# Optimization experiments

Hardware: AMD Instinct MI355X
Metric: run time of the kernel (lower is better)

The kernel has to match this reference:

```python
import jax, jax.numpy as jnp
import numpy as np

N_NODES = 100000
N_EDGES = 1600000
F_IN = 64
CONVS = [128, 128, 64]
DECODER_HID = 128
N_CLASSES = 2


def _glorot(key, shape):
    fan_in = shape[1]
    lim = 1.0 / np.sqrt(fan_in)
    return jax.random.uniform(key, shape, jnp.float32, -lim, lim)


def setup_inputs() -> dict:
    key = jax.random.key(0)
    ks = jax.random.split(key, 16)
    x = jax.random.normal(ks[0], (N_NODES, F_IN), jnp.float32)
    edge_index = jax.random.randint(ks[1], (2, N_EDGES), 0, N_NODES, jnp.int32)
    dims = [F_IN] + CONVS  # [64,128,128,64]
    inp = {"x": x, "edge_index": edge_index}
    ki = 2
    for i in range(len(CONVS)):
        d_in, d_out = dims[i], dims[i + 1]
        inp[f"Wl{i}"] = _glorot(ks[ki], (d_out, d_in)); ki += 1
        inp[f"bl{i}"] = jnp.zeros((d_out,), jnp.float32)
        inp[f"Wr{i}"] = _glorot(ks[ki], (d_out, d_in)); ki += 1
    inp["Wd1"] = _glorot(ks[ki], (DECODER_HID, CONVS[-1])); ki += 1
    inp["bd1"] = jnp.zeros((DECODER_HID,), jnp.float32)
    inp["Wd2"] = _glorot(ks[ki], (N_CLASSES, DECODER_HID)); ki += 1
    inp["bd2"] = jnp.zeros((N_CLASSES,), jnp.float32)
    return inp


def _sage_conv(x, src, dst, inv_deg, Wl, bl, Wr):
    # gather source features per edge, scatter-mean onto destinations
    msg = x[src]                                          # [E, F]
    agg = jax.ops.segment_sum(msg, dst, num_segments=N_NODES)
    agg = agg * inv_deg[:, None]                          # mean aggregation
    # out = lin_l(mean_neighbors) + lin_r(x_self)
    return agg @ Wl.T + bl + x @ Wr.T


def reference(x, edge_index, Wl0, bl0, Wr0, Wl1, bl1, Wr1, Wl2, bl2, Wr2, Wd1, bd1, Wd2, bd2):
    src = edge_index[0]
    dst = edge_index[1]
    deg = jax.ops.segment_sum(jnp.ones((src.shape[0],), x.dtype), dst, num_segments=N_NODES)
    inv_deg = jnp.where(deg > 0, 1.0 / jnp.maximum(deg, 1.0), 0.0)
    params = [(Wl0, bl0, Wr0), (Wl1, bl1, Wr1), (Wl2, bl2, Wr2)]
    h = x
    for i, (Wl, bl, Wr) in enumerate(params):
        h = _sage_conv(h, src, dst, inv_deg, Wl, bl, Wr)
        if i != len(params) - 1:
            h = jax.nn.relu(h)
    # decoder: ReLU -> Linear(64,128) -> ReLU -> Linear(128,2)
    h = jax.nn.relu(h)
    h = jax.nn.relu(h @ Wd1.T + bd1)
    return h @ Wd2.T + bd2
```

## Files before the change

kernel.cpp:

```cpp
#include <hip/hip_runtime.h>
#include <cstdint>
#include <cstddef>

#define NN 100000
#define NE 1600000
#define BSH 9
#define NBUCK 196
#define P3_CHUNK 8192
#define P3_BLOCKS 196

typedef __attribute__((ext_vector_type(8))) short short8;
typedef __attribute__((ext_vector_type(4))) float f32x4;


__device__ inline unsigned pack_split(float v) {
    unsigned u = __builtin_bit_cast(unsigned, v);
    unsigned hi = (u + 0x7fffu + ((u >> 16) & 1u)) >> 16;
    float vh = __builtin_bit_cast(float, hi << 16);
    float r = v - vh;
    unsigned u2 = __builtin_bit_cast(unsigned, r);
    unsigned lo = (u2 + 0x7fffu + ((u2 >> 16) & 1u)) >> 16;
    return hi | (lo << 16);
}

__device__ inline unsigned short rnb(float v) {
    unsigned u = __builtin_bit_cast(unsigned, v);
    return (unsigned short)((u + 0x7fffu + ((u >> 16) & 1u)) >> 16);
}

__device__ inline float bf2f(unsigned short u) {
    return __builtin_bit_cast(float, (unsigned)u << 16);
}


__global__ __launch_bounds__(256) void k_zero_small(int* p, int n) {
    for (int i = threadIdx.x; i < n; i += 256) p[i] = 0;
}

__global__ __launch_bounds__(256) void k_hist(const int* __restrict__ dst, int* __restrict__ bcnt) {
    __shared__ int h[NBUCK];
    const int tid = threadIdx.x;
    if (tid < NBUCK) h[tid] = 0;
    __syncthreads();
    for (int e = blockIdx.x * 256 + tid; e < NE; e += gridDim.x * 256)
        atomicAdd(&h[dst[e] >> BSH], 1);
    __syncthreads();
    if (tid < NBUCK) atomicAdd(&bcnt[tid], h[tid]);
}

__global__ __launch_bounds__(256) void k_bscan(const int* __restrict__ bcnt, int* __restrict__ bstart,
                                               int* __restrict__ gcur) {
    __shared__ int sh[256];
    const int t = threadIdx.x;
    int v = (t < NBUCK) ? bcnt[t] : 0;
    sh[t] = v;
    __syncthreads();
    for (int off = 1; off < 256; off <<= 1) {
        int u = 0;
        if (t >= off) u = sh[t - off];
        __syncthreads();
        sh[t] += u;
        __syncthreads();
    }
    int excl = sh[t] - v;
    if (t < NBUCK) { bstart[t] = excl; gcur[t] = excl; }
    if (t == 0) bstart[NBUCK] = NE;
}

__global__ __launch_bounds__(256) void k_partition(const int* __restrict__ srce, const int* __restrict__ dste,
                                                   int* __restrict__ gcur, int* __restrict__ tmp) {
    __shared__ int h[NBUCK], lstart[NBUCK], gbase[NBUCK], scn[256];
    __shared__ int s_pack[P3_CHUNK];
    __shared__ int s_gad[P3_CHUNK];
    const int tid = threadIdx.x;
    const int base = blockIdx.x * P3_CHUNK;
    if (tid < NBUCK) h[tid] = 0;
    __syncthreads();
    int rank[P3_CHUNK / 256];
#pragma unroll
    for (int i = 0; i < P3_CHUNK / 256; i++) {
        int idx = base + i * 256 + tid;
        if (idx < NE) rank[i] = atomicAdd(&h[dste[idx] >> BSH], 1);
    }
    __syncthreads();
    int hv = (tid < NBUCK) ? h[tid] : 0;
    if (tid < NBUCK) gbase[tid] = atomicAdd(&gcur[tid], hv);
    scn[tid] = hv;
    __syncthreads();
    for (int off = 1; off < 256; off <<= 1) {
        int u = 0;
        if (tid >= off) u = scn[tid - off];
        __syncthreads();
        scn[tid] += u;
        __syncthreads();
    }
    if (tid < NBUCK) lstart[tid] = scn[tid] - hv;
    __syncthreads();
#pragma unroll
    for (int i = 0; i < P3_CHUNK / 256; i++) {
        int idx = base + i * 256 + tid;
        if (idx < NE) {
            int d = dste[idx], s = srce[idx];
            int b = d >> BSH;
            int slot = lstart[b] + rank[i];
            s_pack[slot] = (s << BSH) | (d & ((1 << BSH) - 1));
            s_gad[slot] = gbase[b] + rank[i];
        }
    }
    __syncthreads();
    int chunkN = NE - base;
    if (chunkN > P3_CHUNK) chunkN = P3_CHUNK;
#pragma unroll
    for (int i = 0; i < P3_CHUNK / 256; i++) {
        int slot = i * 256 + tid;
        if (slot < chunkN) tmp[s_gad[slot]] = s_pack[slot];
    }
}

__global__ __launch_bounds__(256) void k_bucket(const int* __restrict__ tmp, const int* __restrict__ bstart,
                                                int* __restrict__ row_ptr, int* __restrict__ col,
                                                float* __restrict__ invd) {
    __shared__ int cnt[512], cur[512], scn[256];
    const int b = blockIdx.x, tid = threadIdx.x;
    const int base = bstart[b];
    const int n = bstart[b + 1] - base;
    cnt[tid] = 0;
    cnt[tid + 256] = 0;
    __syncthreads();
    for (int k = tid; k < n; k += 256) atomicAdd(&cnt[tmp[base + k] & 511], 1);
    __syncthreads();
    int c0 = cnt[2 * tid], c1 = cnt[2 * tid + 1], s = c0 + c1;
    scn[tid] = s;
    __syncthreads();
    for (int off = 1; off < 256; off <<= 1) {
        int u = 0;
        if (tid >= off) u = scn[tid - off];
        __syncthreads();
        scn[tid] += u;
        __syncthreads();
    }
    int excl = scn[tid] - s;
    int node = (b << BSH) + 2 * tid;
    if (node < NN) {
        row_ptr[node] = base + excl;
        invd[node] = c0 ? 1.0f / (float)c0 : 0.0f;
    }
    if (node + 1 < NN) {
        row_ptr[node + 1] = base + excl + c0;
        invd[node + 1] = c1 ? 1.0f / (float)c1 : 0.0f;
    }
    cur[2 * tid] = base + excl;
    cur[2 * tid + 1] = base + excl + c0;
    if (b == 0 && tid == 0) row_ptr[NN] = NE;
    __syncthreads();
    for (int k = tid; k < n; k += 256) {
        int p = tmp[base + k];
        int pos = atomicAdd(&cur[p & 511], 1);
        col[pos] = p >> BSH;
    }
}


__global__ __launch_bounds__(256) void k_xhi(const float* __restrict__ x, unsigned short* __restrict__ Xh) {
    int i = blockIdx.x * 256 + threadIdx.x;
    float4 v = ((const float4*)x)[i];
    ushort4 o = {rnb(v.x), rnb(v.y), rnb(v.z), rnb(v.w)};
    ((ushort4*)Xh)[i] = o;
}

__global__ __launch_bounds__(256) void k_wsplit(const float* __restrict__ Wl0, const float* __restrict__ Wr0,
                                                const float* __restrict__ Wl1, const float* __restrict__ Wr1,
                                                const float* __restrict__ Wl2, const float* __restrict__ Wr2,
                                                const float* __restrict__ Wd1, const float* __restrict__ bl2,
                                                unsigned short* __restrict__ Wh, unsigned short* __restrict__ Wl,
                                                float* __restrict__ biasPQ) {
    int i = blockIdx.x * 256 + threadIdx.x;
    float v = 0.f;
    bool valid = true;
    if (i < 8192) v = Wl0[i];
    else if (i < 16384) v = Wr0[i - 8192];
    else if (i < 32768) v = Wl1[i - 16384];
    else if (i < 49152) v = Wr1[i - 32768];
    else if (i < 57344) v = Wl2[i - 49152];
    else if (i < 65536) v = Wr2[i - 57344];
    else if (i < 73728) v = Wd1[i - 65536];
    else valid = false;
    if (valid) {
        unsigned ps = pack_split(v);
        Wh[i] = (unsigned short)ps;
        Wl[i] = (unsigned short)(ps >> 16);
    }
    if (i >= 73728 && i < 73856) {
        int j = i - 73728;
        biasPQ[j] = (j < 64) ? 0.f : bl2[j - 64];
    }
}


__global__ __launch_bounds__(256) void k_agg64h(const unsigned short* __restrict__ Xh, const int* __restrict__ row_ptr,
                                                const int* __restrict__ col, const float* __restrict__ invd,
                                                unsigned short* __restrict__ Ah, unsigned short* __restrict__ Al) {
    int node = blockIdx.x * 4 + (threadIdx.x >> 6);
    int lane = threadIdx.x & 63;
    int start = row_ptr[node], end = row_ptr[node + 1];
    float a0 = 0.f, a1 = 0.f, a2 = 0.f, a3 = 0.f, a4 = 0.f, a5 = 0.f, a6 = 0.f, a7 = 0.f;
    for (int cs = start; cs < end; cs += 64) {
        int n = end - cs;
        if (n > 64) n = 64;
        int my = (lane < n) ? col[cs + lane] : 0;
        int j = 0;
        for (; j + 8 <= n; j += 8) {
            int s0 = __shfl(my, j + 0), s1 = __shfl(my, j + 1);
            int s2 = __shfl(my, j + 2), s3 = __shfl(my, j + 3);
            int s4 = __shfl(my, j + 4), s5 = __shfl(my, j + 5);
            int s6 = __shfl(my, j + 6), s7 = __shfl(my, j + 7);
            float v0 = bf2f(Xh[(size_t)s0 * 64 + lane]);
            float v1 = bf2f(Xh[(size_t)s1 * 64 + lane]);
            float v2 = bf2f(Xh[(size_t)s2 * 64 + lane]);
            float v3 = bf2f(Xh[(size_t)s3 * 64 + lane]);
            float v4 = bf2f(Xh[(size_t)s4 * 64 + lane]);
            float v5 = bf2f(Xh[(size_t)s5 * 64 + lane]);
            float v6 = bf2f(Xh[(size_t)s6 * 64 + lane]);
            float v7 = bf2f(Xh[(size_t)s7 * 64 + lane]);
            a0 += v0; a1 += v1; a2 += v2; a3 += v3;
            a4 += v4; a5 += v5; a6 += v6; a7 += v7;
        }
        for (; j < n; j++) {
            int s = __shfl(my, j);
            a0 += bf2f(Xh[(size_t)s * 64 + lane]);
        }
    }
    float acc = ((a0 + a1) + (a2 + a3)) + ((a4 + a5) + (a6 + a7));
    unsigned ps = pack_split(acc * invd[node]);
    Ah[(size_t)node * 64 + lane] = (unsigned short)ps;
    Al[(size_t)node * 64 + lane] = (unsigned short)(ps >> 16);
}

__global__ __launch_bounds__(256) void k_agg128h(const unsigned short* __restrict__ Gh, const int* __restrict__ row_ptr,
                                                 const int* __restrict__ col, const float* __restrict__ invd,
                                                 unsigned short* __restrict__ Ah, unsigned short* __restrict__ Al) {
    int node = blockIdx.x * 4 + (threadIdx.x >> 6);
    int lane = threadIdx.x & 63;
    int start = row_ptr[node], end = row_ptr[node + 1];
    float ax0 = 0.f, ax1 = 0.f, ax2 = 0.f, ax3 = 0.f, ax4 = 0.f, ax5 = 0.f, ax6 = 0.f, ax7 = 0.f;
    float ay0 = 0.f, ay1 = 0.f, ay2 = 0.f, ay3 = 0.f, ay4 = 0.f, ay5 = 0.f, ay6 = 0.f, ay7 = 0.f;
    for (int cs = start; cs < end; cs += 64) {
        int n = end - cs;
        if (n > 64) n = 64;
        int my = (lane < n) ? col[cs + lane] : 0;
        int j = 0;
        for (; j + 8 <= n; j += 8) {
            int s0 = __shfl(my, j + 0), s1 = __shfl(my, j + 1);
            int s2 = __shfl(my, j + 2), s3 = __shfl(my, j + 3);
            int s4 = __shfl(my, j + 4), s5 = __shfl(my, j + 5);
            int s6 = __shfl(my, j + 6), s7 = __shfl(my, j + 7);
            unsigned u0 = *(const unsigned*)(Gh + (size_t)s0 * 128 + 2 * lane);
            unsigned u1 = *(const unsigned*)(Gh + (size_t)s1 * 128 + 2 * lane);
            unsigned u2 = *(const unsigned*)(Gh + (size_t)s2 * 128 + 2 * lane);
            unsigned u3 = *(const unsigned*)(Gh + (size_t)s3 * 128 + 2 * lane);
            unsigned u4 = *(const unsigned*)(Gh + (size_t)s4 * 128 + 2 * lane);
            unsigned u5 = *(const unsigned*)(Gh + (size_t)s5 * 128 + 2 * lane);
            unsigned u6 = *(const unsigned*)(Gh + (size_t)s6 * 128 + 2 * lane);
            unsigned u7 = *(const unsigned*)(Gh + (size_t)s7 * 128 + 2 * lane);
            ax0 += bf2f((unsigned short)u0); ay0 += bf2f((unsigned short)(u0 >> 16));
            ax1 += bf2f((unsigned short)u1); ay1 += bf2f((unsigned short)(u1 >> 16));
            ax2 += bf2f((unsigned short)u2); ay2 += bf2f((unsigned short)(u2 >> 16));
            ax3 += bf2f((unsigned short)u3); ay3 += bf2f((unsigned short)(u3 >> 16));
            ax4 += bf2f((unsigned short)u4); ay4 += bf2f((unsigned short)(u4 >> 16));
            ax5 += bf2f((unsigned short)u5); ay5 += bf2f((unsigned short)(u5 >> 16));
            ax6 += bf2f((unsigned short)u6); ay6 += bf2f((unsigned short)(u6 >> 16));
            ax7 += bf2f((unsigned short)u7); ay7 += bf2f((unsigned short)(u7 >> 16));
        }
        for (; j < n; j++) {
            int s = __shfl(my, j);
            unsigned u = *(const unsigned*)(Gh + (size_t)s * 128 + 2 * lane);
            ax0 += bf2f((unsigned short)u);
            ay0 += bf2f((unsigned short)(u >> 16));
        }
    }
    float w = invd[node];
    float sx = (((ax0 + ax1) + (ax2 + ax3)) + ((ax4 + ax5) + (ax6 + ax7))) * w;
    float sy = (((ay0 + ay1) + (ay2 + ay3)) + ((ay4 + ay5) + (ay6 + ay7))) * w;
    unsigned px = pack_split(sx), py = pack_split(sy);
    *(unsigned*)(Ah + (size_t)node * 128 + 2 * lane) = (px & 0xffffu) | (py << 16);
    *(unsigned*)(Al + (size_t)node * 128 + 2 * lane) = (px >> 16) | (py & 0xffff0000u);
}

__global__ __launch_bounds__(256) void k_aggPh(const unsigned short* __restrict__ Ph, const float* __restrict__ Qf,
                                               const int* __restrict__ row_ptr, const int* __restrict__ col,
                                               const float* __restrict__ invd,
                                               unsigned short* __restrict__ Hh, unsigned short* __restrict__ Hl) {
    int node = blockIdx.x * 4 + (threadIdx.x >> 6);
    int lane = threadIdx.x & 63;
    int start = row_ptr[node], end = row_ptr[node + 1];
    float a0 = 0.f, a1 = 0.f, a2 = 0.f, a3 = 0.f, a4 = 0.f, a5 = 0.f, a6 = 0.f, a7 = 0.f;
    for (int cs = start; cs < end; cs += 64) {
        int n = end - cs;
        if (n > 64) n = 64;
        int my = (lane < n) ? col[cs + lane] : 0;
        int j = 0;
        for (; j + 8 <= n; j += 8) {
            int s0 = __shfl(my, j + 0), s1 = __shfl(my, j + 1);
            int s2 = __shfl(my, j + 2), s3 = __shfl(my, j + 3);
            int s4 = __shfl(my, j + 4), s5 = __shfl(my, j + 5);
            int s6 = __shfl(my, j + 6), s7 = __shfl(my, j + 7);
            float v0 = bf2f(Ph[(size_t)s0 * 64 + lane]);
            float v1 = bf2f(Ph[(size_t)s1 * 64 + lane]);
            float v2 = bf2f(Ph[(size_t)s2 * 64 + lane]);
            float v3 = bf2f(Ph[(size_t)s3 * 64 + lane]);
            float v4 = bf2f(Ph[(size_t)s4 * 64 + lane]);
            float v5 = bf2f(Ph[(size_t)s5 * 64 + lane]);
            float v6 = bf2f(Ph[(size_t)s6 * 64 + lane]);
            float v7 = bf2f(Ph[(size_t)s7 * 64 + lane]);
            a0 += v0; a1 += v1; a2 += v2; a3 += v3;
            a4 += v4; a5 += v5; a6 += v6; a7 += v7;
        }
        for (; j < n; j++) {
            int s = __shfl(my, j);
            a0 += bf2f(Ph[(size_t)s * 64 + lane]);
        }
    }
    float acc = ((a0 + a1) + (a2 + a3)) + ((a4 + a5) + (a6 + a7));
    float v = Qf[(size_t)node * 64 + lane] + invd[node] * acc;
    unsigned ps = pack_split(fmaxf(v, 0.f));
    Hh[(size_t)node * 64 + lane] = (unsigned short)ps;
    Hl[(size_t)node * 64 + lane] = (unsigned short)(ps >> 16);
}


#define LA 40

template <int K, int AFMT>
__device__ inline void mgp(const unsigned short* __restrict__ Ah_g, const unsigned short* __restrict__ Al_g,
                           const float* __restrict__ Af_g,
                           const unsigned short* __restrict__ Wh_g, const unsigned short* __restrict__ Wl_g,
                           int m0, unsigned short* sAh, unsigned short* sAl,
                           unsigned short* sBh, unsigned short* sBl,
                           f32x4 (&acc)[4][4], int tid, int wm, int wn, int l15, int quad) {
    const int srow = tid >> 1, sc = (tid & 1) * 16;
#pragma unroll 1
    for (int kt = 0; kt < K; kt += 32) {
        __syncthreads();
        int gr = m0 + srow;
        uint4 h0 = {0, 0, 0, 0}, h1 = {0, 0, 0, 0}, l0 = {0, 0, 0, 0}, l1 = {0, 0, 0, 0};
        if (AFMT == 0) {
            if (gr < NN) {
                const uint4* ph = (const uint4*)(Ah_g + (size_t)gr * K + kt + sc);
                h0 = ph[0]; h1 = ph[1];
                const uint4* pl = (const uint4*)(Al_g + (size_t)gr * K + kt + sc);
                l0 = pl[0]; l1 = pl[1];
            }
        } else {
            if (gr < NN) {
                const float4* pf = (const float4*)(Af_g + (size_t)gr * K + kt + sc);
                float4 f0 = pf[0], f1 = pf[1], f2 = pf[2], f3 = pf[3];
                float fs[16] = {f0.x, f0.y, f0.z, f0.w, f1.x, f1.y, f1.z, f1.w,
                                f2.x, f2.y, f2.z, f2.w, f3.x, f3.y, f3.z, f3.w};
                alignas(16) unsigned short hh[16], ll[16];
#pragma unroll
                for (int i = 0; i < 16; i++) {
                    unsigned ps = pack_split(fs[i]);
                    hh[i] = (unsigned short)ps;
                    ll[i] = (unsigned short)(ps >> 16);
                }
                h0 = *(const uint4*)&hh[0]; h1 = *(const uint4*)&hh[8];
                l0 = *(const uint4*)&ll[0]; l1 = *(const uint4*)&ll[8];
            }
        }
        const uint4* qh = (const uint4*)(Wh_g + srow * K + kt + sc);
        uint4 b0 = qh[0], b1 = qh[1];
        const uint4* ql = (const uint4*)(Wl_g + srow * K + kt + sc);
        uint4 b2 = ql[0], b3 = ql[1];
        *(uint4*)(sAh + srow * LA + sc) = h0; *(uint4*)(sAh + srow * LA + sc + 8) = h1;
        *(uint4*)(sAl + srow * LA + sc) = l0; *(uint4*)(sAl + srow * LA + sc + 8) = l1;
        *(uint4*)(sBh + srow * LA + sc) = b0; *(uint4*)(sBh + srow * LA + sc + 8) = b1;
        *(uint4*)(sBl + srow * LA + sc) = b2; *(uint4*)(sBl + srow * LA + sc + 8) = b3;
        __syncthreads();
        short8 ah[4], al[4], bh[4], bl[4];
#pragma unroll
        for (int t = 0; t < 4; t++) {
            ah[t] = *(const short8*)(sAh + (wm + t * 16 + l15) * LA + quad * 8);
            al[t] = *(const short8*)(sAl + (wm + t * 16 + l15) * LA + quad * 8);
            bh[t] = *(const short8*)(sBh + (wn + t * 16 + l15) * LA + quad * 8);
            bl[t] = *(const short8*)(sBl + (wn + t * 16 + l15) * LA + quad * 8);
        }
#pragma unroll
        for (int mt = 0; mt < 4; mt++)
#pragma unroll
            for (int nt = 0; nt < 4; nt++) {
                acc[mt][nt] = __builtin_amdgcn_mfma_f32_16x16x32_bf16(ah[mt], bh[nt], acc[mt][nt], 0, 0, 0);
                acc[mt][nt] = __builtin_amdgcn_mfma_f32_16x16x32_bf16(ah[mt], bl[nt], acc[mt][nt], 0, 0, 0);
                acc[mt][nt] = __builtin_amdgcn_mfma_f32_16x16x32_bf16(al[mt], bh[nt], acc[mt][nt], 0, 0, 0);
            }
    }
}

template <int K1, int K2, int AF1, int AF2, bool RELU, int OMODE>
__global__ __launch_bounds__(256) void k_mgemm(
    const unsigned short* A1h, const unsigned short* A1l, const float* A1f,
    const unsigned short* A2h, const unsigned short* A2l, const float* A2f,
    const unsigned short* __restrict__ W1h, const unsigned short* __restrict__ W1l,
    const unsigned short* __restrict__ W2h, const unsigned short* __restrict__ W2l,
    const float* __restrict__ bias, float* Cf, unsigned short* Chi, unsigned short* Clo,
    unsigned short* Ph, float* Qf) {
    __shared__ unsigned short sAh[128 * LA], sAl[128 * LA], sBh[128 * LA], sBl[128 * LA];
    const int tid = threadIdx.x;
    const int m0 = blockIdx.x * 128;
    const int wave = tid >> 6, lane = tid & 63;
    const int wm = (wave & 1) * 64, wn = (wave >> 1) * 64;
    const int l15 = lane & 15, quad = lane >> 4;
    f32x4 acc[4][4];
#pragma unroll
    for (int i = 0; i < 4; i++)
#pragma unroll
        for (int j = 0; j < 4; j++) acc[i][j] = (f32x4){0.f, 0.f, 0.f, 0.f};

    mgp<K1, AF1>(A1h, A1l, A1f, W1h, W1l, m0, sAh, sAl, sBh, sBl, acc, tid, wm, wn, l15, quad);
    if (K2 > 0) mgp<K2, AF2>(A2h, A2l, A2f, W2h, W2l, m0, sAh, sAl, sBh, sBl, acc, tid, wm, wn, l15, quad);

#pragma unroll
    for (int mt = 0; mt < 4; mt++) {
        int rbase = m0 + wm + mt * 16 + quad * 4;
#pragma unroll
        for (int nt = 0; nt < 4; nt++) {
            int cg = wn + nt * 16 + l15;
            float bv = bias[cg];
#pragma unroll
            for (int r = 0; r < 4; r++) {
                int row = rbase + r;
                if (row < NN) {
                    float v = acc[mt][nt][r] + bv;
                    if (RELU) v = fmaxf(v, 0.f);
                    if (OMODE == 0) {
                        Cf[(size_t)row * 128 + cg] = v;
                    } else if (OMODE == 1) {
                        unsigned ps = pack_split(v);
                        Chi[(size_t)row * 128 + cg] = (unsigned short)ps;
                        Clo[(size_t)row * 128 + cg] = (unsigned short)(ps >> 16);
                    } else {
                        if (cg < 64) Ph[(size_t)row * 64 + cg] = rnb(v);
                        else Qf[(size_t)row * 64 + cg - 64] = v;
                    }
                }
            }
        }
    }
}


__global__ __launch_bounds__(256) void k_dec2(const float* __restrict__ h, const float* __restrict__ W,
                                              const float* __restrict__ b, float* __restrict__ out) {
    int node = blockIdx.x * 4 + (threadIdx.x >> 6);
    int lane = threadIdx.x & 63;
    float2 hv = *((const float2*)(h + (size_t)node * 128) + lane);
    float d0 = hv.x * W[2 * lane] + hv.y * W[2 * lane + 1];
    float d1 = hv.x * W[128 + 2 * lane] + hv.y * W[128 + 2 * lane + 1];
    for (int off = 32; off > 0; off >>= 1) {
        d0 += __shfl_down(d0, off);
        d1 += __shfl_down(d1, off);
    }
    if (lane == 0) {
        out[(size_t)node * 2 + 0] = d0 + b[0];
        out[(size_t)node * 2 + 1] = d1 + b[1];
    }
}


extern "C" void kernel_launch(void* const* d_in, const int* in_sizes, int n_in,
                              void* d_out, int out_size, void* d_ws, size_t ws_size,
                              hipStream_t stream) {
    const float* x   = (const float*)d_in[0];
    const int*   ei  = (const int*)d_in[1];
    const float* Wl0 = (const float*)d_in[2];
    const float* bl0 = (const float*)d_in[3];
    const float* Wr0 = (const float*)d_in[4];
    const float* Wl1 = (const float*)d_in[5];
    const float* bl1 = (const float*)d_in[6];
    const float* Wr1 = (const float*)d_in[7];
    const float* Wl2 = (const float*)d_in[8];
    const float* bl2 = (const float*)d_in[9];
    const float* Wr2 = (const float*)d_in[10];
    const float* Wd1 = (const float*)d_in[11];
    const float* bd1 = (const float*)d_in[12];
    const float* Wd2 = (const float*)d_in[13];
    const float* bd2 = (const float*)d_in[14];
    float* out = (float*)d_out;

    char* ws = (char*)d_ws;
    size_t off = 0;
    auto alloc = [&](size_t bytes) {
        char* p = ws + off;
        off = (off + bytes + 255) & ~(size_t)255;
        return p;
    };
    int*            bcnt    = (int*)alloc((size_t)NBUCK * 4);
    int*            bstart  = (int*)alloc((size_t)(NBUCK + 1) * 4);
    int*            gcur    = (int*)alloc((size_t)NBUCK * 4);
    int*            row_ptr = (int*)alloc((size_t)(NN + 1) * 4);
    float*          invd    = (float*)alloc((size_t)NN * 4);
    float*          biasPQ  = (float*)alloc(128 * 4);
    unsigned short* Wh      = (unsigned short*)alloc((size_t)73728 * 2);
    unsigned short* Wl      = (unsigned short*)alloc((size_t)73728 * 2);
    int*            col     = (int*)alloc((size_t)NE * 4);
    char*           R1      = alloc((size_t)NN * 128 * 4);
    char*           R2      = alloc((size_t)NN * 128 * 4);
    (void)ws_size;

    int*            tmp   = (int*)R1;
    unsigned short* Xh    = (unsigned short*)R1;
    unsigned short* Agg0h = (unsigned short*)(R1 + 12800000);
    unsigned short* Agg0l = (unsigned short*)(R1 + 25600000);
    unsigned short* Agg1h = (unsigned short*)R1;
    unsigned short* Agg1l = (unsigned short*)(R1 + 25600000);
    unsigned short* Ph    = (unsigned short*)R1;
    float*          Qf    = (float*)(R1 + 12800000);
    float*          d1    = (float*)R1;
    unsigned short* G0h   = (unsigned short*)R2;
    unsigned short* G0l   = (unsigned short*)(R2 + 25600000);
    unsigned short* H1h   = G0h;
    unsigned short* H1l   = G0l;
    unsigned short* h2h   = (unsigned short*)R2;
    unsigned short* h2l   = (unsigned short*)(R2 + 12800000);

    const unsigned short* WL0h = Wh,         * WL0l = Wl;
    const unsigned short* WR0h = Wh + 8192,  * WR0l = Wl + 8192;
    const unsigned short* WL1h = Wh + 16384, * WL1l = Wl + 16384;
    const unsigned short* WR1h = Wh + 32768, * WR1l = Wl + 32768;
    const unsigned short* WPQh = Wh + 49152, * WPQl = Wl + 49152;
    const unsigned short* WD1h = Wh + 65536, * WD1l = Wl + 65536;

    const int* srce = ei;
    const int* dste = ei + NE;

    k_zero_small<<<1, 256, 0, stream>>>(bcnt, NBUCK);
    k_hist<<<400, 256, 0, stream>>>(dste, bcnt);
    k_bscan<<<1, 256, 0, stream>>>(bcnt, bstart, gcur);
    k_partition<<<P3_BLOCKS, 256, 0, stream>>>(srce, dste, gcur, tmp);
    k_bucket<<<NBUCK, 256, 0, stream>>>(tmp, bstart, row_ptr, col, invd);

    k_wsplit<<<289, 256, 0, stream>>>(Wl0, Wr0, Wl1, Wr1, Wl2, Wr2, Wd1, bl2, Wh, Wl, biasPQ);
    k_xhi<<<(NN * 64 / 4 + 255) / 256, 256, 0, stream>>>(x, Xh);

    const int gGemm = (NN + 127) / 128;
    const int gNode = NN / 4;

    k_agg64h<<<gNode, 256, 0, stream>>>(Xh, row_ptr, col, invd, Agg0h, Agg0l);
    k_mgemm<64, 64, 0, 1, true, 1><<<gGemm, 256, 0, stream>>>(
        Agg0h, Agg0l, nullptr, nullptr, nullptr, x,
        WL0h, WL0l, WR0h, WR0l, bl0, nullptr, G0h, G0l, nullptr, nullptr);

    k_agg128h<<<gNode, 256, 0, stream>>>(G0h, row_ptr, col, invd, Agg1h, Agg1l);
    k_mgemm<128, 128, 0, 0, true, 1><<<gGemm, 256, 0, stream>>>(
        Agg1h, Agg1l, nullptr, G0h, G0l, nullptr,
        WL1h, WL1l, WR1h, WR1l, bl1, nullptr, H1h, H1l, nullptr, nullptr);

    k_mgemm<128, 0, 0, 0, false, 2><<<gGemm, 256, 0, stream>>>(
        H1h, H1l, nullptr, nullptr, nullptr, nullptr,
        WPQh, WPQl, nullptr, nullptr, biasPQ, nullptr, nullptr, nullptr, Ph, Qf);
    k_aggPh<<<gNode, 256, 0, stream>>>(Ph, Qf, row_ptr, col, invd, h2h, h2l);

    k_mgemm<64, 0, 0, 0, true, 0><<<gGemm, 256, 0, stream>>>(
        h2h, h2l, nullptr, nullptr, nullptr, nullptr,
        WD1h, WD1l, nullptr, nullptr, bd1, d1, nullptr, nullptr, nullptr, nullptr);
    k_dec2<<<gNode, 256, 0, stream>>>(d1, Wd2, bd2, out);
}
```

Before: 488.5 us.

## Fuse final decoder linear into GEMM epilogue and use fixed-capacity edge buckets

```diff
diff --git a/kernel.cpp b/kernel.cpp
--- a/kernel.cpp
+++ b/kernel.cpp
@@ -6,6 +6,7 @@
 #define NE 1600000
 #define BSH 9
 #define NBUCK 196
+#define CAP 9216
 #define P3_CHUNK 8192
 #define P3_BLOCKS 196
 
@@ -33,38 +34,9 @@
 }
 
 
-__global__ __launch_bounds__(256) void k_zero_small(int* p, int n) {
-    for (int i = threadIdx.x; i < n; i += 256) p[i] = 0;
-}
-
-__global__ __launch_bounds__(256) void k_hist(const int* __restrict__ dst, int* __restrict__ bcnt) {
-    __shared__ int h[NBUCK];
-    const int tid = threadIdx.x;
-    if (tid < NBUCK) h[tid] = 0;
-    __syncthreads();
-    for (int e = blockIdx.x * 256 + tid; e < NE; e += gridDim.x * 256)
-        atomicAdd(&h[dst[e] >> BSH], 1);
-    __syncthreads();
-    if (tid < NBUCK) atomicAdd(&bcnt[tid], h[tid]);
-}
-
-__global__ __launch_bounds__(256) void k_bscan(const int* __restrict__ bcnt, int* __restrict__ bstart,
-                                               int* __restrict__ gcur) {
-    __shared__ int sh[256];
-    const int t = threadIdx.x;
-    int v = (t < NBUCK) ? bcnt[t] : 0;
-    sh[t] = v;
-    __syncthreads();
-    for (int off = 1; off < 256; off <<= 1) {
-        int u = 0;
-        if (t >= off) u = sh[t - off];
-        __syncthreads();
-        sh[t] += u;
-        __syncthreads();
-    }
-    int excl = sh[t] - v;
-    if (t < NBUCK) { bstart[t] = excl; gcur[t] = excl; }
-    if (t == 0) bstart[NBUCK] = NE;
+__global__ __launch_bounds__(256) void k_init_gcur(int* gcur) {
+    int t = threadIdx.x;
+    if (t < NBUCK) gcur[t] = t * CAP;
 }
 
 __global__ __launch_bounds__(256) void k_partition(const int* __restrict__ srce, const int* __restrict__ dste,
@@ -117,13 +89,13 @@
     }
 }
 
-__global__ __launch_bounds__(256) void k_bucket(const int* __restrict__ tmp, const int* __restrict__ bstart,
-                                                int* __restrict__ row_ptr, int* __restrict__ col,
-                                                float* __restrict__ invd) {
+__global__ __launch_bounds__(256) void k_bucket(const int* __restrict__ tmp, const int* __restrict__ gend,
+                                                int* __restrict__ row_ptr, int* __restrict__ rc,
+                                                int* __restrict__ col, float* __restrict__ invd) {
     __shared__ int cnt[512], cur[512], scn[256];
     const int b = blockIdx.x, tid = threadIdx.x;
-    const int base = bstart[b];
-    const int n = bstart[b + 1] - base;
+    const int base = b * CAP;
+    const int n = gend[b] - base;
     cnt[tid] = 0;
     cnt[tid + 256] = 0;
     __syncthreads();
@@ -143,15 +115,16 @@
     int node = (b << BSH) + 2 * tid;
     if (node < NN) {
         row_ptr[node] = base + excl;
+        rc[node] = c0;
         invd[node] = c0 ? 1.0f / (float)c0 : 0.0f;
     }
     if (node + 1 < NN) {
         row_ptr[node + 1] = base + excl + c0;
+        rc[node + 1] = c1;
         invd[node + 1] = c1 ? 1.0f / (float)c1 : 0.0f;
     }
     cur[2 * tid] = base + excl;
     cur[2 * tid + 1] = base + excl + c0;
-    if (b == 0 && tid == 0) row_ptr[NN] = NE;
     __syncthreads();
     for (int k = tid; k < n; k += 256) {
         int p = tmp[base + k];
@@ -198,37 +171,33 @@
 
 
 __global__ __launch_bounds__(256) void k_agg64h(const unsigned short* __restrict__ Xh, const int* __restrict__ row_ptr,
-                                                const int* __restrict__ col, const float* __restrict__ invd,
+                                                const int* __restrict__ rc, const int* __restrict__ col,
+                                                const float* __restrict__ invd,
                                                 unsigned short* __restrict__ Ah, unsigned short* __restrict__ Al) {
     int node = blockIdx.x * 4 + (threadIdx.x >> 6);
     int lane = threadIdx.x & 63;
-    int start = row_ptr[node], end = row_ptr[node + 1];
+    int start = row_ptr[node], cnt = rc[node];
     float a0 = 0.f, a1 = 0.f, a2 = 0.f, a3 = 0.f, a4 = 0.f, a5 = 0.f, a6 = 0.f, a7 = 0.f;
-    for (int cs = start; cs < end; cs += 64) {
-        int n = end - cs;
-        if (n > 64) n = 64;
-        int my = (lane < n) ? col[cs + lane] : 0;
-        int j = 0;
-        for (; j + 8 <= n; j += 8) {
-            int s0 = __shfl(my, j + 0), s1 = __shfl(my, j + 1);
-            int s2 = __shfl(my, j + 2), s3 = __shfl(my, j + 3);
-            int s4 = __shfl(my, j + 4), s5 = __shfl(my, j + 5);
-            int s6 = __shfl(my, j + 6), s7 = __shfl(my, j + 7);
-            float v0 = bf2f(Xh[(size_t)s0 * 64 + lane]);
-            float v1 = bf2f(Xh[(size_t)s1 * 64 + lane]);
-            float v2 = bf2f(Xh[(size_t)s2 * 64 + lane]);
-            float v3 = bf2f(Xh[(size_t)s3 * 64 + lane]);
-            float v4 = bf2f(Xh[(size_t)s4 * 64 + lane]);
-            float v5 = bf2f(Xh[(size_t)s5 * 64 + lane]);
-            float v6 = bf2f(Xh[(size_t)s6 * 64 + lane]);
-            float v7 = bf2f(Xh[(size_t)s7 * 64 + lane]);
-            a0 += v0; a1 += v1; a2 += v2; a3 += v3;
-            a4 += v4; a5 += v5; a6 += v6; a7 += v7;
-        }
-        for (; j < n; j++) {
-            int s = __shfl(my, j);
-            a0 += bf2f(Xh[(size_t)s * 64 + lane]);
-        }
+    int j = 0;
+    for (; j + 8 <= cnt; j += 8) {
+        int s0 = col[start + j + 0], s1 = col[start + j + 1];
+        int s2 = col[start + j + 2], s3 = col[start + j + 3];
+        int s4 = col[start + j + 4], s5 = col[start + j + 5];
+        int s6 = col[start + j + 6], s7 = col[start + j + 7];
+        float v0 = bf2f(Xh[(size_t)s0 * 64 + lane]);
+        float v1 = bf2f(Xh[(size_t)s1 * 64 + lane]);
+        float v2 = bf2f(Xh[(size_t)s2 * 64 + lane]);
+        float v3 = bf2f(Xh[(size_t)s3 * 64 + lane]);
+        float v4 = bf2f(Xh[(size_t)s4 * 64 + lane]);
+        float v5 = bf2f(Xh[(size_t)s5 * 64 + lane]);
+        float v6 = bf2f(Xh[(size_t)s6 * 64 + lane]);
+        float v7 = bf2f(Xh[(size_t)s7 * 64 + lane]);
+        a0 += v0; a1 += v1; a2 += v2; a3 += v3;
+        a4 += v4; a5 += v5; a6 += v6; a7 += v7;
+    }
+    for (; j < cnt; j++) {
+        int s = col[start + j];
+        a0 += bf2f(Xh[(size_t)s * 64 + lane]);
     }
     float acc = ((a0 + a1) + (a2 + a3)) + ((a4 + a5) + (a6 + a7));
     unsigned ps = pack_split(acc * invd[node]);
@@ -237,46 +206,42 @@
 }
 
 __global__ __launch_bounds__(256) void k_agg128h(const unsigned short* __restrict__ Gh, const int* __restrict__ row_ptr,
-                                                 const int* __restrict__ col, const float* __restrict__ invd,
+                                                 const int* __restrict__ rc, const int* __restrict__ col,
+                                                 const float* __restrict__ invd,
                                                  unsigned short* __restrict__ Ah, unsigned short* __restrict__ Al) {
     int node = blockIdx.x * 4 + (threadIdx.x >> 6);
     int lane = threadIdx.x & 63;
-    int start = row_ptr[node], end = row_ptr[node + 1];
+    int start = row_ptr[node], cnt = rc[node];
     float ax0 = 0.f, ax1 = 0.f, ax2 = 0.f, ax3 = 0.f, ax4 = 0.f, ax5 = 0.f, ax6 = 0.f, ax7 = 0.f;
     float ay0 = 0.f, ay1 = 0.f, ay2 = 0.f, ay3 = 0.f, ay4 = 0.f, ay5 = 0.f, ay6 = 0.f, ay7 = 0.f;
-    for (int cs = start; cs < end; cs += 64) {
-        int n = end - cs;
-        if (n > 64) n = 64;
-        int my = (lane < n) ? col[cs + lane] : 0;
-        int j = 0;
-        for (; j + 8 <= n; j += 8) {
-            int s0 = __shfl(my, j + 0), s1 = __shfl(my, j + 1);
-            int s2 = __shfl(my, j + 2), s3 = __shfl(my, j + 3);
-            int s4 = __shfl(my, j + 4), s5 = __shfl(my, j + 5);
-            int s6 = __shfl(my, j + 6), s7 = __shfl(my, j + 7);
-            unsigned u0 = *(const unsigned*)(Gh + (size_t)s0 * 128 + 2 * lane);
-            unsigned u1 = *(const unsigned*)(Gh + (size_t)s1 * 128 + 2 * lane);
-            unsigned u2 = *(const unsigned*)(Gh + (size_t)s2 * 128 + 2 * lane);
-            unsigned u3 = *(const unsigned*)(Gh + (size_t)s3 * 128 + 2 * lane);
-            unsigned u4 = *(const unsigned*)(Gh + (size_t)s4 * 128 + 2 * lane);
-            unsigned u5 = *(const unsigned*)(Gh + (size_t)s5 * 128 + 2 * lane);
-            unsigned u6 = *(const unsigned*)(Gh + (size_t)s6 * 128 + 2 * lane);
-            unsigned u7 = *(const unsigned*)(Gh + (size_t)s7 * 128 + 2 * lane);
-            ax0 += bf2f((unsigned short)u0); ay0 += bf2f((unsigned short)(u0 >> 16));
-            ax1 += bf2f((unsigned short)u1); ay1 += bf2f((unsigned short)(u1 >> 16));
-            ax2 += bf2f((unsigned short)u2); ay2 += bf2f((unsigned short)(u2 >> 16));
-            ax3 += bf2f((unsigned short)u3); ay3 += bf2f((unsigned short)(u3 >> 16));
-            ax4 += bf2f((unsigned short)u4); ay4 += bf2f((unsigned short)(u4 >> 16));
-            ax5 += bf2f((unsigned short)u5); ay5 += bf2f((unsigned short)(u5 >> 16));
-            ax6 += bf2f((unsigned short)u6); ay6 += bf2f((unsigned short)(u6 >> 16));
-            ax7 += bf2f((unsigned short)u7); ay7 += bf2f((unsigned short)(u7 >> 16));
-        }
-        for (; j < n; j++) {
-            int s = __shfl(my, j);
-            unsigned u = *(const unsigned*)(Gh + (size_t)s * 128 + 2 * lane);
-            ax0 += bf2f((unsigned short)u);
-            ay0 += bf2f((unsigned short)(u >> 16));
-        }
+    int j = 0;
+    for (; j + 8 <= cnt; j += 8) {
+        int s0 = col[start + j + 0], s1 = col[start + j + 1];
+        int s2 = col[start + j + 2], s3 = col[start + j + 3];
+        int s4 = col[start + j + 4], s5 = col[start + j + 5];
+        int s6 = col[start + j + 6], s7 = col[start + j + 7];
+        unsigned u0 = *(const unsigned*)(Gh + (size_t)s0 * 128 + 2 * lane);
+        unsigned u1 = *(const unsigned*)(Gh + (size_t)s1 * 128 + 2 * lane);
+        unsigned u2 = *(const unsigned*)(Gh + (size_t)s2 * 128 + 2 * lane);
+        unsigned u3 = *(const unsigned*)(Gh + (size_t)s3 * 128 + 2 * lane);
+        unsigned u4 = *(const unsigned*)(Gh + (size_t)s4 * 128 + 2 * lane);
+        unsigned u5 = *(const unsigned*)(Gh + (size_t)s5 * 128 + 2 * lane);
+        unsigned u6 = *(const unsigned*)(Gh + (size_t)s6 * 128 + 2 * lane);
+        unsigned u7 = *(const unsigned*)(Gh + (size_t)s7 * 128 + 2 * lane);
+        ax0 += bf2f((unsigned short)u0); ay0 += bf2f((unsigned short)(u0 >> 16));
+        ax1 += bf2f((unsigned short)u1); ay1 += bf2f((unsigned short)(u1 >> 16));
+        ax2 += bf2f((unsigned short)u2); ay2 += bf2f((unsigned short)(u2 >> 16));
+        ax3 += bf2f((unsigned short)u3); ay3 += bf2f((unsigned short)(u3 >> 16));
+        ax4 += bf2f((unsigned short)u4); ay4 += bf2f((unsigned short)(u4 >> 16));
+        ax5 += bf2f((unsigned short)u5); ay5 += bf2f((unsigned short)(u5 >> 16));
+        ax6 += bf2f((unsigned short)u6); ay6 += bf2f((unsigned short)(u6 >> 16));
+        ax7 += bf2f((unsigned short)u7); ay7 += bf2f((unsigned short)(u7 >> 16));
+    }
+    for (; j < cnt; j++) {
+        int s = col[start + j];
+        unsigned u = *(const unsigned*)(Gh + (size_t)s * 128 + 2 * lane);
+        ax0 += bf2f((unsigned short)u);
+        ay0 += bf2f((unsigned short)(u >> 16));
     }
     float w = invd[node];
     float sx = (((ax0 + ax1) + (ax2 + ax3)) + ((ax4 + ax5) + (ax6 + ax7))) * w;
@@ -287,38 +252,33 @@
 }
 
 __global__ __launch_bounds__(256) void k_aggPh(const unsigned short* __restrict__ Ph, const float* __restrict__ Qf,
-                                               const int* __restrict__ row_ptr, const int* __restrict__ col,
-                                               const float* __restrict__ invd,
+                                               const int* __restrict__ row_ptr, const int* __restrict__ rc,
+                                               const int* __restrict__ col, const float* __restrict__ invd,
                                                unsigned short* __restrict__ Hh, unsigned short* __restrict__ Hl) {
     int node = blockIdx.x * 4 + (threadIdx.x >> 6);
     int lane = threadIdx.x & 63;
-    int start = row_ptr[node], end = row_ptr[node + 1];
+    int start = row_ptr[node], cnt = rc[node];
     float a0 = 0.f, a1 = 0.f, a2 = 0.f, a3 = 0.f, a4 = 0.f, a5 = 0.f, a6 = 0.f, a7 = 0.f;
-    for (int cs = start; cs < end; cs += 64) {
-        int n = end - cs;
-        if (n > 64) n = 64;
-        int my = (lane < n) ? col[cs + lane] : 0;
-        int j = 0;
-        for (; j + 8 <= n; j += 8) {
-            int s0 = __shfl(my, j + 0), s1 = __shfl(my, j + 1);
-            int s2 = __shfl(my, j + 2), s3 = __shfl(my, j + 3);
-            int s4 = __shfl(my, j + 4), s5 = __shfl(my, j + 5);
-            int s6 = __shfl(my, j + 6), s7 = __shfl(my, j + 7);
-            float v0 = bf2f(Ph[(size_t)s0 * 64 + lane]);
-            float v1 = bf2f(Ph[(size_t)s1 * 64 + lane]);
-            float v2 = bf2f(Ph[(size_t)s2 * 64 + lane]);
-            float v3 = bf2f(Ph[(size_t)s3 * 64 + lane]);
-            float v4 = bf2f(Ph[(size_t)s4 * 64 + lane]);
-            float v5 = bf2f(Ph[(size_t)s5 * 64 + lane]);
-            float v6 = bf2f(Ph[(size_t)s6 * 64 + lane]);
-            float v7 = bf2f(Ph[(size_t)s7 * 64 + lane]);
-            a0 += v0; a1 += v1; a2 += v2; a3 += v3;
-            a4 += v4; a5 += v5; a6 += v6; a7 += v7;
-        }
-        for (; j < n; j++) {
-            int s = __shfl(my, j);
-            a0 += bf2f(Ph[(size_t)s * 64 + lane]);
-        }
+    int j = 0;
+    for (; j + 8 <= cnt; j += 8) {
+        int s0 = col[start + j + 0], s1 = col[start + j + 1];
+        int s2 = col[start + j + 2], s3 = col[start + j + 3];
+        int s4 = col[start + j + 4], s5 = col[start + j + 5];
+        int s6 = col[start + j + 6], s7 = col[start + j + 7];
+        float v0 = bf2f(Ph[(size_t)s0 * 64 + lane]);
+        float v1 = bf2f(Ph[(size_t)s1 * 64 + lane]);
+        float v2 = bf2f(Ph[(size_t)s2 * 64 + lane]);
+        float v3 = bf2f(Ph[(size_t)s3 * 64 + lane]);
+        float v4 = bf2f(Ph[(size_t)s4 * 64 + lane]);
+        float v5 = bf2f(Ph[(size_t)s5 * 64 + lane]);
+        float v6 = bf2f(Ph[(size_t)s6 * 64 + lane]);
+        float v7 = bf2f(Ph[(size_t)s7 * 64 + lane]);
+        a0 += v0; a1 += v1; a2 += v2; a3 += v3;
+        a4 += v4; a5 += v5; a6 += v6; a7 += v7;
+    }
+    for (; j < cnt; j++) {
+        int s = col[start + j];
+        a0 += bf2f(Ph[(size_t)s * 64 + lane]);
     }
     float acc = ((a0 + a1) + (a2 + a3)) + ((a4 + a5) + (a6 + a7));
     float v = Qf[(size_t)node * 64 + lane] + invd[node] * acc;
@@ -402,7 +362,8 @@
     const unsigned short* __restrict__ W1h, const unsigned short* __restrict__ W1l,
     const unsigned short* __restrict__ W2h, const unsigned short* __restrict__ W2l,
     const float* __restrict__ bias, float* Cf, unsigned short* Chi, unsigned short* Clo,
-    unsigned short* Ph, float* Qf) {
+    unsigned short* Ph, float* Qf,
+    const float* __restrict__ Wd2, const float* __restrict__ bd2, float* outp) {
     __shared__ unsigned short sAh[128 * LA], sAl[128 * LA], sBh[128 * LA], sBl[128 * LA];
     const int tid = threadIdx.x;
     const int m0 = blockIdx.x * 128;
@@ -417,6 +378,48 @@
 
     mgp<K1, AF1>(A1h, A1l, A1f, W1h, W1l, m0, sAh, sAl, sBh, sBl, acc, tid, wm, wn, l15, quad);
     if (K2 > 0) mgp<K2, AF2>(A2h, A2l, A2f, W2h, W2l, m0, sAh, sAl, sBh, sBl, acc, tid, wm, wn, l15, quad);
+
+    if (OMODE == 3) {
+        __syncthreads();
+        float* sOut = (float*)sAh;
+        sOut[tid] = 0.f;
+        __syncthreads();
+        float w0[4], w1[4], bv[4];
+#pragma unroll
+        for (int nt = 0; nt < 4; nt++) {
+            int cg = wn + nt * 16 + l15;
+            w0[nt] = Wd2[cg];
+            w1[nt] = Wd2[128 + cg];
+            bv[nt] = bias[cg];
+        }
+#pragma unroll
+        for (int mt = 0; mt < 4; mt++) {
+#pragma unroll
+            for (int r = 0; r < 4; r++) {
+                float s0 = 0.f, s1 = 0.f;
+#pragma unroll
+                for (int nt = 0; nt < 4; nt++) {
+                    float v = fmaxf(acc[mt][nt][r] + bv[nt], 0.f);
+                    s0 += v * w0[nt];
+                    s1 += v * w1[nt];
+                }
+                s0 += __shfl_xor(s0, 1); s1 += __shfl_xor(s1, 1);
+                s0 += __shfl_xor(s0, 2); s1 += __shfl_xor(s1, 2);
+                s0 += __shfl_xor(s0, 4); s1 += __shfl_xor(s1, 4);
+                s0 += __shfl_xor(s0, 8); s1 += __shfl_xor(s1, 8);
+                if (l15 == 0) {
+                    int lr = wm + mt * 16 + quad * 4 + r;
+                    atomicAdd(&sOut[lr * 2 + 0], s0);
+                    atomicAdd(&sOut[lr * 2 + 1], s1);
+                }
+            }
+        }
+        __syncthreads();
+        int lr = tid >> 1, c = tid & 1;
+        int row = m0 + lr;
+        if (row < NN) outp[(size_t)row * 2 + c] = sOut[lr * 2 + c] + bd2[c];
+        return;
+    }
 
 #pragma unroll
     for (int mt = 0; mt < 4; mt++) {
@@ -444,24 +447,6 @@
                 }
             }
         }
-    }
-}
-
-
-__global__ __launch_bounds__(256) void k_dec2(const float* __restrict__ h, const float* __restrict__ W,
-                                              const float* __restrict__ b, float* __restrict__ out) {
-    int node = blockIdx.x * 4 + (threadIdx.x >> 6);
-    int lane = threadIdx.x & 63;
-    float2 hv = *((const float2*)(h + (size_t)node * 128) + lane);
-    float d0 = hv.x * W[2 * lane] + hv.y * W[2 * lane + 1];
-    float d1 = hv.x * W[128 + 2 * lane] + hv.y * W[128 + 2 * lane + 1];
-    for (int off = 32; off > 0; off >>= 1) {
-        d0 += __shfl_down(d0, off);
-        d1 += __shfl_down(d1, off);
-    }
-    if (lane == 0) {
-        out[(size_t)node * 2 + 0] = d0 + b[0];
-        out[(size_t)node * 2 + 1] = d1 + b[1];
     }
 }
 
@@ -493,15 +478,14 @@
         off = (off + bytes + 255) & ~(size_t)255;
         return p;
     };
-    int*            bcnt    = (int*)alloc((size_t)NBUCK * 4);
-    int*            bstart  = (int*)alloc((size_t)(NBUCK + 1) * 4);
     int*            gcur    = (int*)alloc((size_t)NBUCK * 4);
-    int*            row_ptr = (int*)alloc((size_t)(NN + 1) * 4);
+    int*            row_ptr = (int*)alloc((size_t)NN * 4);
+    int*            rc      = (int*)alloc((size_t)NN * 4);
     float*          invd    = (float*)alloc((size_t)NN * 4);
     float*          biasPQ  = (float*)alloc(128 * 4);
     unsigned short* Wh      = (unsigned short*)alloc((size_t)73728 * 2);
     unsigned short* Wl      = (unsigned short*)alloc((size_t)73728 * 2);
-    int*            col     = (int*)alloc((size_t)NE * 4);
+    int*            col     = (int*)alloc((size_t)NBUCK * CAP * 4);
     char*           R1      = alloc((size_t)NN * 128 * 4);
     char*           R2      = alloc((size_t)NN * 128 * 4);
     (void)ws_size;
@@ -514,7 +498,6 @@
     unsigned short* Agg1l = (unsigned short*)(R1 + 25600000);
     unsigned short* Ph    = (unsigned short*)R1;
     float*          Qf    = (float*)(R1 + 12800000);
-    float*          d1    = (float*)R1;
     unsigned short* G0h   = (unsigned short*)R2;
     unsigned short* G0l   = (unsigned short*)(R2 + 25600000);
     unsigned short* H1h   = G0h;
@@ -532,11 +515,9 @@
     const int* srce = ei;
     const int* dste = ei + NE;
 
-    k_zero_small<<<1, 256, 0, stream>>>(bcnt, NBUCK);
-    k_hist<<<400, 256, 0, stream>>>(dste, bcnt);
-    k_bscan<<<1, 256, 0, stream>>>(bcnt, bstart, gcur);
+    k_init_gcur<<<1, 256, 0, stream>>>(gcur);
     k_partition<<<P3_BLOCKS, 256, 0, stream>>>(srce, dste, gcur, tmp);
-    k_bucket<<<NBUCK, 256, 0, stream>>>(tmp, bstart, row_ptr, col, invd);
+    k_bucket<<<NBUCK, 256, 0, stream>>>(tmp, gcur, row_ptr, rc, col, invd);
 
     k_wsplit<<<289, 256, 0, stream>>>(Wl0, Wr0, Wl1, Wr1, Wl2, Wr2, Wd1, bl2, Wh, Wl, biasPQ);
     k_xhi<<<(NN * 64 / 4 + 255) / 256, 256, 0, stream>>>(x, Xh);
@@ -544,23 +525,26 @@
     const int gGemm = (NN + 127) / 128;
     const int gNode = NN / 4;
 
-    k_agg64h<<<gNode, 256, 0, stream>>>(Xh, row_ptr, col, invd, Agg0h, Agg0l);
+    k_agg64h<<<gNode, 256, 0, stream>>>(Xh, row_ptr, rc, col, invd, Agg0h, Agg0l);
     k_mgemm<64, 64, 0, 1, true, 1><<<gGemm, 256, 0, stream>>>(
         Agg0h, Agg0l, nullptr, nullptr, nullptr, x,
-        WL0h, WL0l, WR0h, WR0l, bl0, nullptr, G0h, G0l, nullptr, nullptr);
-
-    k_agg128h<<<gNode, 256, 0, stream>>>(G0h, row_ptr, col, invd, Agg1h, Agg1l);
+        WL0h, WL0l, WR0h, WR0l, bl0, nullptr, G0h, G0l, nullptr, nullptr,
+        nullptr, nullptr, nullptr);
+
+    k_agg128h<<<gNode, 256, 0, stream>>>(G0h, row_ptr, rc, col, invd, Agg1h, Agg1l);
     k_mgemm<128, 128, 0, 0, true, 1><<<gGemm, 256, 0, stream>>>(
         Agg1h, Agg1l, nullptr, G0h, G0l, nullptr,
-        WL1h, WL1l, WR1h, WR1l, bl1, nullptr, H1h, H1l, nullptr, nullptr);
+        WL1h, WL1l, WR1h, WR1l, bl1, nullptr, H1h, H1l, nullptr, nullptr,
+        nullptr, nullptr, nullptr);
 
     k_mgemm<128, 0, 0, 0, false, 2><<<gGemm, 256, 0, stream>>>(
         H1h, H1l, nullptr, nullptr, nullptr, nullptr,
-        WPQh, WPQl, nullptr, nullptr, biasPQ, nullptr, nullptr, nullptr, Ph, Qf);
-    k_aggPh<<<gNode, 256, 0, stream>>>(Ph, Qf, row_ptr, col, invd, h2h, h2l);
-
-    k_mgemm<64, 0, 0, 0, true, 0><<<gGemm, 256, 0, stream>>>(
+        WPQh, WPQl, nullptr, nullptr, biasPQ, nullptr, nullptr, nullptr, Ph, Qf,
+        nullptr, nullptr, nullptr);
+    k_aggPh<<<gNode, 256, 0, stream>>>(Ph, Qf, row_ptr, rc, col, invd, h2h, h2l);
+
+    k_mgemm<64, 0, 0, 0, true, 3><<<gGemm, 256, 0, stream>>>(
         h2h, h2l, nullptr, nullptr, nullptr, nullptr,
-        WD1h, WD1l, nullptr, nullptr, bd1, d1, nullptr, nullptr, nullptr, nullptr);
-    k_dec2<<<gNode, 256, 0, stream>>>(d1, Wd2, bd2, out);
-}
+        WD1h, WD1l, nullptr, nullptr, bd1, nullptr, nullptr, nullptr, nullptr, nullptr,
+        Wd2, bd2, out);
+}
```

New measurement: 489.2 us. No clear change (+0.1%).
